# Optimization experiments

Measured on AMD Instinct MI355X. Metric: run time of the kernel, lower is better.

## Reference

```python
import jax, jax.numpy as jnp
import numpy as np

H = 128
N_CAN = 100000
N_FLAG = 50000
E = 600000
L = 500000


def _sage_conv(x_src, x_dst, edge_index, Wl, bl, Wr):
    # PyG SAGEConv (mean aggr): lin_l(mean_{j in N(i)} x_j) + lin_r(x_i)
    src, dst = edge_index[0], edge_index[1]
    msg = x_src[src]                                        # [E, H] gather
    n_dst = x_dst.shape[0]
    agg = jax.ops.segment_sum(msg, dst, num_segments=n_dst)  # [N_dst, H]
    cnt = jax.ops.segment_sum(jnp.ones((msg.shape[0],), msg.dtype), dst,
                              num_segments=n_dst)
    mean = agg / jnp.maximum(cnt, 1.0)[:, None]
    return mean @ Wl.T + bl + x_dst @ Wr.T


def setup_inputs() -> dict:
    key = jax.random.key(0)
    ks = jax.random.split(key, 16)
    s = 1.0 / np.sqrt(H)
    inp = {
        'can_node_id': jnp.arange(N_CAN, dtype=jnp.int64) if jax.config.jax_enable_x64 else jnp.arange(N_CAN, dtype=jnp.int32),
        'flag_node_id': jnp.arange(N_FLAG, dtype=jnp.int32),
        'edge_index_cf': jnp.stack([
            jax.random.randint(ks[0], (E,), 0, N_CAN),
            jax.random.randint(ks[1], (E,), 0, N_FLAG)]),
        'edge_index_fc': jnp.stack([
            jax.random.randint(ks[2], (E,), 0, N_FLAG),
            jax.random.randint(ks[3], (E,), 0, N_CAN)]),
        'edge_label_index': jnp.stack([
            jax.random.randint(ks[4], (L,), 0, N_CAN),
            jax.random.randint(ks[5], (L,), 0, N_FLAG)]),
        'can_emb': jax.random.normal(ks[6], (N_CAN, H), jnp.float32),
        'flag_emb': jax.random.normal(ks[7], (N_FLAG, H), jnp.float32),
        # SAGEConv for edge type CAN->flag (updates flag nodes)
        'Wl_cf': jax.random.normal(ks[8], (H, H), jnp.float32) * s,
        'bl_cf': jnp.zeros((H,), jnp.float32),
        'Wr_cf': jax.random.normal(ks[9], (H, H), jnp.float32) * s,
        # SAGEConv for edge type flag->CAN (updates CAN nodes)
        'Wl_fc': jax.random.normal(ks[10], (H, H), jnp.float32) * s,
        'bl_fc': jnp.zeros((H,), jnp.float32),
        'Wr_fc': jax.random.normal(ks[11], (H, H), jnp.float32) * s,
        # classifier MLP
        'W1': jax.random.normal(ks[12], (H, 2 * H), jnp.float32) * (1.0 / np.sqrt(2 * H)),
        'b1': jnp.zeros((H,), jnp.float32),
        'W2': jax.random.normal(ks[13], (1, H), jnp.float32) * s,
        'b2': jnp.zeros((1,), jnp.float32),
    }
    return inp


def reference(can_node_id, flag_node_id, edge_index_cf, edge_index_fc,
              edge_label_index, can_emb, flag_emb,
              Wl_cf, bl_cf, Wr_cf, Wl_fc, bl_fc, Wr_fc,
              W1, b1, W2, b2):
    # embedding lookups
    x_can = can_emb[can_node_id]    # [N_CAN, H]
    x_flag = flag_emb[flag_node_id]  # [N_FLAG, H]
    # to_hetero single SAGE layer + relu (dropout is identity in eval)
    upd_flag = jax.nn.relu(_sage_conv(x_can, x_flag, edge_index_cf, Wl_cf, bl_cf, Wr_cf))
    upd_can = jax.nn.relu(_sage_conv(x_flag, x_can, edge_index_fc, Wl_fc, bl_fc, Wr_fc))
    # link prediction classifier
    src = upd_can[edge_label_index[0]]   # [L, H]
    dst = upd_flag[edge_label_index[1]]  # [L, H]
    h = jax.nn.relu(jnp.concatenate([src, dst], axis=-1) @ W1.T + b1)
    out = h @ W2.T + b2
    return out.reshape(-1)
```

## Files before the change

### kernel.cpp

```cpp
#include <hip/hip_runtime.h>
#include <hip/hip_bf16.h>

#define H 128
#define BSH 8
#define MAXB 1024

typedef __attribute__((ext_vector_type(8))) short short8;
typedef __attribute__((ext_vector_type(4))) short short4v;
typedef __attribute__((ext_vector_type(4))) float floatx4;
typedef unsigned short ushort_t;
typedef unsigned int uint_t;

__device__ __forceinline__ short f2bf(float f) {
    __hip_bfloat16 h = __float2bfloat16(f);
    return *reinterpret_cast<short*>(&h);
}
__device__ __forceinline__ float bflo(uint_t u) { return __uint_as_float(u << 16); }
__device__ __forceinline__ float bfhi(uint_t u) { return __uint_as_float(u & 0xFFFF0000u); }
__device__ __forceinline__ uint_t pack_bf2(float x, float y) {
    return (uint_t)(ushort_t)f2bf(x) | ((uint_t)(ushort_t)f2bf(y) << 16);
}

__global__ __launch_bounds__(256)
void bucket_hist_cvt_kernel(const int* __restrict__ ei1, const int* __restrict__ ei2,
                            int E, int NF, int B, int* __restrict__ bcnt, int nbh,
                            const float* __restrict__ a, int n4a,
                            const float* __restrict__ b, int n4b,
                            ushort_t* __restrict__ da, ushort_t* __restrict__ db,
                            const float* __restrict__ Wl_cf, const float* __restrict__ Wr_cf,
                            const float* __restrict__ Wl_fc, const float* __restrict__ Wr_fc,
                            const float* __restrict__ W1, ushort_t* __restrict__ wb) {
    __shared__ int h[MAXB];
    int tid = threadIdx.x;
    if ((int)blockIdx.x < nbh) {
        for (int i = tid; i < B; i += 256) h[i] = 0;
        __syncthreads();
        int base = blockIdx.x * 4096;
        #pragma unroll 4
        for (int it = 0; it < 16; ++it) {
            int t = base + it * 256 + tid;
            if (t < 2 * E) {
                int g = (t < E) ? ei1[E + t] : (ei2[E + t - E] + NF);
                atomicAdd(&h[g >> BSH], 1);
            }
        }
        __syncthreads();
        for (int i = tid; i < B; i += 256)
            if (h[i]) atomicAdd(&bcnt[i], h[i]);
        return;
    }
    int i = ((int)blockIdx.x - nbh) * 256 + tid;
    const float* src; ushort_t* dst; int k;
    if (i < n4a) { src = a; dst = da; k = i; }
    else if (i < n4a + n4b) { src = b; dst = db; k = i - n4a; }
    else {
        int idx = (i - n4a - n4b) * 4;
        if (idx >= 98304) return;
        int off;
        if      (idx < 16384) { src = Wl_cf; off = idx; }
        else if (idx < 32768) { src = Wr_cf; off = idx - 16384; }
        else if (idx < 49152) { src = Wl_fc; off = idx - 32768; }
        else if (idx < 65536) { src = Wr_fc; off = idx - 49152; }
        else                  { src = W1;    off = idx - 65536; }
        float4 v = *(const float4*)(src + off);
        short4v s;
        s[0] = f2bf(v.x); s[1] = f2bf(v.y); s[2] = f2bf(v.z); s[3] = f2bf(v.w);
        *(short4v*)(wb + idx) = s;
        return;
    }
    float4 v = ((const float4*)src)[k];
    short4v s;
    s[0] = f2bf(v.x); s[1] = f2bf(v.y); s[2] = f2bf(v.z); s[3] = f2bf(v.w);
    ((short4v*)dst)[k] = s;
}

__global__ __launch_bounds__(256)
void bucket_scan_kernel(const int* __restrict__ bcnt, int B,
                        int* __restrict__ bbase, int* __restrict__ bfront) {
    __shared__ int sdata[256];
    int tid = threadIdx.x;
    int base = tid * 4;
    int v[4]; int s = 0;
    #pragma unroll
    for (int i = 0; i < 4; ++i) { int idx = base + i; v[i] = (idx < B) ? bcnt[idx] : 0; s += v[i]; }
    sdata[tid] = s;
    __syncthreads();
    for (int off = 1; off < 256; off <<= 1) {
        int t = (tid >= off) ? sdata[tid - off] : 0;
        __syncthreads();
        sdata[tid] += t;
        __syncthreads();
    }
    int excl = tid ? sdata[tid - 1] : 0;
    #pragma unroll
    for (int i = 0; i < 4; ++i) {
        int idx = base + i;
        if (idx < B) { bbase[idx] = excl; bfront[idx] = excl; }
        excl += v[i];
    }
    if (tid == 255) bbase[B] = excl;
}

__global__ __launch_bounds__(256)
void partition_kernel(const int* __restrict__ ei1, const int* __restrict__ ei2,
                      int E, int NF, int B,
                      int* __restrict__ bfront, uint2* __restrict__ part) {
    __shared__ int h[MAXB];
    __shared__ int basex[MAXB];
    int tid = threadIdx.x;
    for (int i = tid; i < B; i += 256) h[i] = 0;
    __syncthreads();
    int base = blockIdx.x * 4096;
    #pragma unroll 4
    for (int it = 0; it < 16; ++it) {
        int t = base + it * 256 + tid;
        if (t < 2 * E) {
            int g = (t < E) ? ei1[E + t] : (ei2[E + t - E] + NF);
            atomicAdd(&h[g >> BSH], 1);
        }
    }
    __syncthreads();
    for (int i = tid; i < B; i += 256) {
        int c = h[i];
        basex[i] = c ? atomicAdd(&bfront[i], c) : 0;
    }
    __syncthreads();
    for (int i = tid; i < B; i += 256) h[i] = 0;
    __syncthreads();
    #pragma unroll 4
    for (int it = 0; it < 16; ++it) {
        int t = base + it * 256 + tid;
        if (t < 2 * E) {
            int g, s;
            if (t < E) { g = ei1[E + t]; s = ei1[t]; }
            else       { int e = t - E; g = ei2[E + e] + NF; s = ei2[e]; }
            int bk = g >> BSH;
            int r = atomicAdd(&h[bk], 1);
            part[basex[bk] + r] = make_uint2((uint_t)s, (uint_t)g);
        }
    }
}

__global__ __launch_bounds__(256)
void fine_bin_kernel(const int* __restrict__ bbase, int nTot,
                     const uint2* __restrict__ part,
                     int* __restrict__ offs, int* __restrict__ bins) {
    __shared__ int cnt[256];
    __shared__ int sdata[256];
    __shared__ int excl[256];
    int b = blockIdx.x;
    int tid = threadIdx.x;
    int seg0 = bbase[b], seg1 = bbase[b + 1];
    int gbase = b << BSH;
    cnt[tid] = 0;
    __syncthreads();
    for (int k = seg0 + tid; k < seg1; k += 256)
        atomicAdd(&cnt[part[k].y - gbase], 1);
    __syncthreads();
    sdata[tid] = cnt[tid];
    __syncthreads();
    for (int off = 1; off < 256; off <<= 1) {
        int t = (tid >= off) ? sdata[tid - off] : 0;
        __syncthreads();
        sdata[tid] += t;
        __syncthreads();
    }
    excl[tid] = tid ? sdata[tid - 1] : 0;
    int g = gbase + tid;
    if (g < nTot) offs[g] = seg0 + excl[tid];
    if (b == (int)gridDim.x - 1 && tid == 0) offs[nTot] = seg1;
    cnt[tid] = 0;
    __syncthreads();
    for (int k = seg0 + tid; k < seg1; k += 256) {
        uint2 e = part[k];
        int l = (int)e.y - gbase;
        int r = atomicAdd(&cnt[l], 1);
        bins[seg0 + excl[l] + r] = (int)e.x;
    }
}

__global__ __launch_bounds__(256)
void gather_mean3_kernel(const int* __restrict__ offs, int nTotal, int split,
                         const int* __restrict__ bins,
                         const ushort_t* __restrict__ embA, ushort_t* __restrict__ aggA,
                         const ushort_t* __restrict__ embB, ushort_t* __restrict__ aggB) {
    int g = blockIdx.x * 4 + (threadIdx.x >> 6);
    if (g >= nTotal) return;
    int lane = threadIdx.x & 63;
    int q = lane >> 4, l15 = lane & 15;
    int start = offs[g];
    int end = offs[g + 1];
    int deg = end - start;
    const ushort_t* emb; ushort_t* agg; int row;
    if (g < split) { emb = embA; agg = aggA; row = g; }
    else           { emb = embB; agg = aggB; row = g - split; }

    float acc[8];
    #pragma unroll
    for (int t = 0; t < 8; ++t) acc[t] = 0.f;

    int nPre = deg < 64 ? deg : 64;
    int pre = (lane < nPre) ? bins[start + lane] : 0;

    int col = l15 * 8;
    for (int it = 0; it < (nPre + 7) / 8; ++it) {
        int e0 = 8 * it + q;
        int e1 = e0 + 4;
        int s0 = __shfl(pre, e0, 64);
        int s1 = __shfl(pre, e1, 64);
        if (e0 < nPre) {
            uint4 r = *(const uint4*)(emb + (size_t)s0 * H + col);
            acc[0] += bflo(r.x); acc[1] += bfhi(r.x);
            acc[2] += bflo(r.y); acc[3] += bfhi(r.y);
            acc[4] += bflo(r.z); acc[5] += bfhi(r.z);
            acc[6] += bflo(r.w); acc[7] += bfhi(r.w);
        }
        if (e1 < nPre) {
            uint4 r = *(const uint4*)(emb + (size_t)s1 * H + col);
            acc[0] += bflo(r.x); acc[1] += bfhi(r.x);
            acc[2] += bflo(r.y); acc[3] += bfhi(r.y);
            acc[4] += bflo(r.z); acc[5] += bfhi(r.z);
            acc[6] += bflo(r.w); acc[7] += bfhi(r.w);
        }
    }
    for (int k = start + 64 + q; k < end; k += 4) {
        int s = bins[k];
        uint4 r = *(const uint4*)(emb + (size_t)s * H + col);
        acc[0] += bflo(r.x); acc[1] += bfhi(r.x);
        acc[2] += bflo(r.y); acc[3] += bfhi(r.y);
        acc[4] += bflo(r.z); acc[5] += bfhi(r.z);
        acc[6] += bflo(r.w); acc[7] += bfhi(r.w);
    }

    #pragma unroll
    for (int t = 0; t < 8; ++t) {
        acc[t] += __shfl_xor(acc[t], 16, 64);
        acc[t] += __shfl_xor(acc[t], 32, 64);
    }
    if (q == 0) {
        float inv = 1.0f / fmaxf((float)deg, 1.0f);
        uint4 o;
        o.x = pack_bf2(acc[0] * inv, acc[1] * inv);
        o.y = pack_bf2(acc[2] * inv, acc[3] * inv);
        o.z = pack_bf2(acc[4] * inv, acc[5] * inv);
        o.w = pack_bf2(acc[6] * inv, acc[7] * inv);
        *(uint4*)(agg + (size_t)row * H + col) = o;
    }
}

__global__ __launch_bounds__(256)
void hist2_kernel(const int* __restrict__ ei1, const int* __restrict__ ei2, int E,
                  int* __restrict__ deg1, int* __restrict__ deg2) {
    int t = blockIdx.x * 256 + threadIdx.x;
    if (t < E) atomicAdd(&deg1[ei1[E + t]], 1);
    else if (t < 2 * E) { int e = t - E; atomicAdd(&deg2[ei2[E + e]], 1); }
}

__global__ __launch_bounds__(256)
void scan_blocksum_kernel(const int* __restrict__ deg, int n, int* __restrict__ bsums) {
    __shared__ int sdata[256];
    int tid = threadIdx.x;
    int base = blockIdx.x * 1024 + tid * 4;
    int v = 0;
    #pragma unroll
    for (int i = 0; i < 4; ++i) { int idx = base + i; if (idx < n) v += deg[idx]; }
    sdata[tid] = v;
    __syncthreads();
    for (int off = 128; off > 0; off >>= 1) {
        if (tid < off) sdata[tid] += sdata[tid + off];
        __syncthreads();
    }
    if (tid == 0) bsums[blockIdx.x] = sdata[0];
}

__global__ __launch_bounds__(256)
void scan_write_kernel(int* __restrict__ data, int n, const int* __restrict__ bsums) {
    __shared__ int sdata[256];
    __shared__ int boff;
    int tid = threadIdx.x;
    if (tid < 64) {
        int acc = 0;
        for (int i = tid; i < (int)blockIdx.x; i += 64) acc += bsums[i];
        #pragma unroll
        for (int off = 32; off > 0; off >>= 1) acc += __shfl_xor(acc, off, 64);
        if (tid == 0) boff = acc;
    }
    int base = blockIdx.x * 1024 + tid * 4;
    int v[4]; int s = 0;
    #pragma unroll
    for (int i = 0; i < 4; ++i) { int idx = base + i; v[i] = (idx < n) ? data[idx] : 0; s += v[i]; }
    sdata[tid] = s;
    __syncthreads();
    for (int off = 1; off < 256; off <<= 1) {
        int t = (tid >= off) ? sdata[tid - off] : 0;
        __syncthreads();
        sdata[tid] += t;
        __syncthreads();
    }
    int excl = (tid == 0 ? 0 : sdata[tid - 1]) + boff;
    #pragma unroll
    for (int i = 0; i < 4; ++i) {
        int idx = base + i;
        if (idx < n) data[idx] = excl;
        excl += v[i];
    }
}

__global__ __launch_bounds__(256)
void bin2_kernel(const int* __restrict__ ei1, const int* __restrict__ ei2, int E,
                 int* __restrict__ offs1, int* __restrict__ offs2,
                 int* __restrict__ bins) {
    int t = blockIdx.x * 256 + threadIdx.x;
    if (t < E) {
        int pos = atomicAdd(&offs1[ei1[E + t]], 1);
        bins[pos] = ei1[t];
    } else if (t < 2 * E) {
        int e = t - E;
        int pos = atomicAdd(&offs2[ei2[E + e]], 1);
        bins[pos] = ei2[e];
    }
}

__global__ __launch_bounds__(256)
void gather_mean2_incl_kernel(const int* __restrict__ offs, int nTotal, int split,
                              const int* __restrict__ bins,
                              const ushort_t* __restrict__ embA, ushort_t* __restrict__ aggA,
                              const ushort_t* __restrict__ embB, ushort_t* __restrict__ aggB) {
    int g = blockIdx.x * 4 + (threadIdx.x >> 6);
    if (g >= nTotal) return;
    int lane = threadIdx.x & 63;
    int q = lane >> 4, l15 = lane & 15;
    int end = offs[g];
    int start = (g == 0) ? 0 : offs[g - 1];
    int deg = end - start;
    const ushort_t* emb; ushort_t* agg; int row;
    if (g < split) { emb = embA; agg = aggA; row = g; }
    else           { emb = embB; agg = aggB; row = g - split; }
    float acc[8];
    #pragma unroll
    for (int t = 0; t < 8; ++t) acc[t] = 0.f;
    int nPre = deg < 64 ? deg : 64;
    int pre = (lane < nPre) ? bins[start + lane] : 0;
    int col = l15 * 8;
    for (int it = 0; it < (nPre + 7) / 8; ++it) {
        int e0 = 8 * it + q, e1 = e0 + 4;
        int s0 = __shfl(pre, e0, 64);
        int s1 = __shfl(pre, e1, 64);
        if (e0 < nPre) {
            uint4 r = *(const uint4*)(emb + (size_t)s0 * H + col);
            acc[0] += bflo(r.x); acc[1] += bfhi(r.x);
            acc[2] += bflo(r.y); acc[3] += bfhi(r.y);
            acc[4] += bflo(r.z); acc[5] += bfhi(r.z);
            acc[6] += bflo(r.w); acc[7] += bfhi(r.w);
        }
        if (e1 < nPre) {
            uint4 r = *(const uint4*)(emb + (size_t)s1 * H + col);
            acc[0] += bflo(r.x); acc[1] += bfhi(r.x);
            acc[2] += bflo(r.y); acc[3] += bfhi(r.y);
            acc[4] += bflo(r.z); acc[5] += bfhi(r.z);
            acc[6] += bflo(r.w); acc[7] += bfhi(r.w);
        }
    }
    for (int k = start + 64 + q; k < end; k += 4) {
        int s = bins[k];
        uint4 r = *(const uint4*)(emb + (size_t)s * H + col);
        acc[0] += bflo(r.x); acc[1] += bfhi(r.x);
        acc[2] += bflo(r.y); acc[3] += bfhi(r.y);
        acc[4] += bflo(r.z); acc[5] += bfhi(r.z);
        acc[6] += bflo(r.w); acc[7] += bfhi(r.w);
    }
    #pragma unroll
    for (int t = 0; t < 8; ++t) {
        acc[t] += __shfl_xor(acc[t], 16, 64);
        acc[t] += __shfl_xor(acc[t], 32, 64);
    }
    if (q == 0) {
        float inv = 1.0f / fmaxf((float)deg, 1.0f);
        uint4 o;
        o.x = pack_bf2(acc[0] * inv, acc[1] * inv);
        o.y = pack_bf2(acc[2] * inv, acc[3] * inv);
        o.z = pack_bf2(acc[4] * inv, acc[5] * inv);
        o.w = pack_bf2(acc[6] * inv, acc[7] * inv);
        *(uint4*)(agg + (size_t)row * H + col) = o;
    }
}

__global__ __launch_bounds__(256)
void sage2_kernel(int nbF, int NF, int NC,
                  ushort_t* __restrict__ aggf, const ushort_t* __restrict__ embf,
                  ushort_t* __restrict__ aggc, const ushort_t* __restrict__ embc,
                  const ushort_t* __restrict__ wlf, const ushort_t* __restrict__ wrf,
                  const float* __restrict__ blf,
                  const ushort_t* __restrict__ wlc, const ushort_t* __restrict__ wrc,
                  const float* __restrict__ blc,
                  const ushort_t* __restrict__ W1) {
    __shared__ short A[64][264];
    bool isF = (int)blockIdx.x < nbF;
    int nrows = isF ? NF : NC;
    int rbase = (isF ? blockIdx.x : blockIdx.x - nbF) * 64;
    ushort_t* io = isF ? aggf : aggc;
    const ushort_t* emb = isF ? embf : embc;
    const ushort_t* Wl = isF ? wlf : wlc;
    const ushort_t* Wr = isF ? wrf : wrc;
    const float* bl = isF ? blf : blc;
    int koff = isF ? 128 : 0;

    int tid = threadIdx.x;
    int lane = tid & 63;
    int wv = tid >> 6;
    int l15 = lane & 15;
    int quad = lane >> 4;
    int nb0 = 32 * wv + l15;

    for (int idx = tid; idx < 64 * 64; idx += 256) {
        int r = idx >> 6, qq = idx & 63;
        int row = rbase + r;
        short4v s = (short4v){0, 0, 0, 0};
        if (row < nrows) {
            const ushort_t* src = (qq < 32) ? (io + (size_t)row * H + qq * 4)
                                            : (emb + (size_t)row * H + (qq - 32) * 4);
            s = *(const short4v*)src;
        }
        *(short4v*)&A[r][qq * 4] = s;
    }

    floatx4 acc[4][2];
    #pragma unroll
    for (int i = 0; i < 4; ++i)
        #pragma unroll
        for (int j = 0; j < 2; ++j)
            acc[i][j] = (floatx4){0.f, 0.f, 0.f, 0.f};

    float blv0 = bl[nb0];
    float blv1 = bl[nb0 + 16];
    __syncthreads();

    #pragma unroll
    for (int half = 0; half < 2; ++half) {
        const ushort_t* W = half ? Wr : Wl;
        #pragma unroll
        for (int ks = 0; ks < 4; ++ks) {
            int kb = ks * 32 + quad * 8;
            short8 b0 = *(const short8*)(W + (size_t)nb0 * H + kb);
            short8 b1 = *(const short8*)(W + (size_t)(nb0 + 16) * H + kb);
            int ka = half * 128 + kb;
            #pragma unroll
            for (int mt = 0; mt < 4; ++mt) {
                short8 a = *(const short8*)&A[16 * mt + l15][ka];
                acc[mt][0] = __builtin_amdgcn_mfma_f32_16x16x32_bf16(a, b0, acc[mt][0], 0, 0, 0);
                acc[mt][1] = __builtin_amdgcn_mfma_f32_16x16x32_bf16(a, b1, acc[mt][1], 0, 0, 0);
            }
        }
    }

    __syncthreads();
    #pragma unroll
    for (int mt = 0; mt < 4; ++mt)
        #pragma unroll
        for (int nt = 0; nt < 2; ++nt) {
            float blv = nt ? blv1 : blv0;
            int colw = nb0 + 16 * nt;
            #pragma unroll
            for (int rg = 0; rg < 4; ++rg) {
                int row = 16 * mt + quad * 4 + rg;
                A[row][colw] = f2bf(fmaxf(acc[mt][nt][rg] + blv, 0.0f));
                acc[mt][nt][rg] = 0.0f;
            }
        }
    __syncthreads();

    const ushort_t* W1p = W1 + koff;
    #pragma unroll
    for (int ks = 0; ks < 4; ++ks) {
        int kb = ks * 32 + quad * 8;
        short8 b0 = *(const short8*)(W1p + (size_t)nb0 * 256 + kb);
        short8 b1 = *(const short8*)(W1p + (size_t)(nb0 + 16) * 256 + kb);
        #pragma unroll
        for (int mt = 0; mt < 4; ++mt) {
            short8 a = *(const short8*)&A[16 * mt + l15][kb];
            acc[mt][0] = __builtin_amdgcn_mfma_f32_16x16x32_bf16(a, b0, acc[mt][0], 0, 0, 0);
            acc[mt][1] = __builtin_amdgcn_mfma_f32_16x16x32_bf16(a, b1, acc[mt][1], 0, 0, 0);
        }
    }

    #pragma unroll
    for (int mt = 0; mt < 4; ++mt)
        #pragma unroll
        for (int rg = 0; rg < 4; ++rg) {
            int row = rbase + 16 * mt + quad * 4 + rg;
            if (row < nrows) {
                io[(size_t)row * H + nb0]      = (ushort_t)f2bf(acc[mt][0][rg]);
                io[(size_t)row * H + nb0 + 16] = (ushort_t)f2bf(acc[mt][1][rg]);
            }
        }
}

__global__ __launch_bounds__(256)
void classify_kernel(const int* __restrict__ eli, int L,
                     const ushort_t* __restrict__ u_can,
                     const ushort_t* __restrict__ u_flag,
                     const float* __restrict__ b1,
                     const float* __restrict__ W2,
                     const float* __restrict__ b2,
                     float* __restrict__ out) {
    int tid = threadIdx.x;
    int lane = tid & 63;
    int wv = tid >> 6;
    int sub = lane >> 4;
    int l15 = lane & 15;
    int p = blockIdx.x * 16 + wv * 4 + sub;
    if (p >= L) return;
    int i = eli[p];
    int j = eli[L + p];
    uint4 a = ((const uint4*)(u_can  + (size_t)i * H))[l15];
    uint4 b = ((const uint4*)(u_flag + (size_t)j * H))[l15];
    float4 bb0 = ((const float4*)b1)[l15 * 2];
    float4 bb1 = ((const float4*)b1)[l15 * 2 + 1];
    float4 w0  = ((const float4*)W2)[l15 * 2];
    float4 w1  = ((const float4*)W2)[l15 * 2 + 1];
    float s = fmaxf(bflo(a.x) + bflo(b.x) + bb0.x, 0.f) * w0.x
            + fmaxf(bfhi(a.x) + bfhi(b.x) + bb0.y, 0.f) * w0.y
            + fmaxf(bflo(a.y) + bflo(b.y) + bb0.z, 0.f) * w0.z
            + fmaxf(bfhi(a.y) + bfhi(b.y) + bb0.w, 0.f) * w0.w
            + fmaxf(bflo(a.z) + bflo(b.z) + bb1.x, 0.f) * w1.x
            + fmaxf(bfhi(a.z) + bfhi(b.z) + bb1.y, 0.f) * w1.y
            + fmaxf(bflo(a.w) + bflo(b.w) + bb1.z, 0.f) * w1.z
            + fmaxf(bfhi(a.w) + bfhi(b.w) + bb1.w, 0.f) * w1.w;
    #pragma unroll
    for (int off = 8; off > 0; off >>= 1)
        s += __shfl_down(s, off, 16);
    if (l15 == 0) out[p] = s + b2[0];
}

extern "C" void kernel_launch(void* const* d_in, const int* in_sizes, int n_in,
                              void* d_out, int out_size, void* d_ws, size_t ws_size,
                              hipStream_t stream) {
    const int*   ei_cf    = (const int*)d_in[2];
    const int*   ei_fc    = (const int*)d_in[3];
    const int*   eli      = (const int*)d_in[4];
    const float* can_emb  = (const float*)d_in[5];
    const float* flag_emb = (const float*)d_in[6];
    const float* Wl_cf    = (const float*)d_in[7];
    const float* bl_cf    = (const float*)d_in[8];
    const float* Wr_cf    = (const float*)d_in[9];
    const float* Wl_fc    = (const float*)d_in[10];
    const float* bl_fc    = (const float*)d_in[11];
    const float* Wr_fc    = (const float*)d_in[12];
    const float* W1       = (const float*)d_in[13];
    const float* b1       = (const float*)d_in[14];
    const float* W2       = (const float*)d_in[15];
    const float* b2       = (const float*)d_in[16];
    float* out = (float*)d_out;

    const int NCAN  = in_sizes[0];
    const int NFLAG = in_sizes[1];
    const int E     = in_sizes[2] / 2;
    const int L     = in_sizes[4] / 2;
    const int nTot  = NCAN + NFLAG;
    const int B     = (nTot + 255) >> BSH;

    ushort_t* aggc = (ushort_t*)d_ws;
    ushort_t* aggf = aggc + (size_t)NCAN * H;
    ushort_t* embc = aggf + (size_t)NFLAG * H;
    ushort_t* embf = embc + (size_t)NCAN * H;
    char* tail = (char*)(embf + (size_t)NFLAG * H);
    size_t tail_off = (size_t)(tail - (char*)d_ws);

    int nbF = (NFLAG + 63) / 64, nbC = (NCAN + 63) / 64;
    int n4c = NCAN * H / 4, n4f = NFLAG * H / 4;
    int nbcvt = (n4c + n4f + 24576 + 255) / 256;

    size_t off_offs  = tail_off;
    size_t off_bcnt  = off_offs  + (size_t)(nTot + 1) * 4;
    size_t off_bbase = off_bcnt  + (size_t)MAXB * 4;
    size_t off_bfrnt = off_bbase + (size_t)(MAXB + 1) * 4;
    size_t off_bins  = off_bfrnt + (size_t)MAXB * 4;
    size_t off_part  = (off_bins + (size_t)2 * E * 4 + 7) & ~(size_t)7;
    size_t off_wb    = off_part + (size_t)2 * E * 8;
    size_t need_new  = off_wb + 98304 * 2;

    if (ws_size >= need_new && B <= MAXB) {
        int* offs   = (int*)((char*)d_ws + off_offs);
        int* bcnt   = (int*)((char*)d_ws + off_bcnt);
        int* bbase  = (int*)((char*)d_ws + off_bbase);
        int* bfront = (int*)((char*)d_ws + off_bfrnt);
        int* bins   = (int*)((char*)d_ws + off_bins);
        uint2* part = (uint2*)((char*)d_ws + off_part);
        ushort_t* wb = (ushort_t*)((char*)d_ws + off_wb);
        ushort_t* wb_wlcf = wb, *wb_wrcf = wb + 16384, *wb_wlfc = wb + 32768,
                 *wb_wrfc = wb + 49152, *wb_w1 = wb + 65536;

        int nbh = (2 * E + 4095) >> 12;
        hipMemsetAsync(bcnt, 0, (size_t)MAXB * 4, stream);
        bucket_hist_cvt_kernel<<<nbh + nbcvt, 256, 0, stream>>>(
            ei_cf, ei_fc, E, NFLAG, B, bcnt, nbh,
            can_emb, n4c, flag_emb, n4f, embc, embf,
            Wl_cf, Wr_cf, Wl_fc, Wr_fc, W1, wb);
        bucket_scan_kernel<<<1, 256, 0, stream>>>(bcnt, B, bbase, bfront);
        partition_kernel<<<nbh, 256, 0, stream>>>(ei_cf, ei_fc, E, NFLAG, B, bfront, part);
        fine_bin_kernel<<<B, 256, 0, stream>>>(bbase, nTot, part, offs, bins);
        gather_mean3_kernel<<<(nTot + 3) / 4, 256, 0, stream>>>(
            offs, nTot, NFLAG, bins, embc, aggf, embf, aggc);
        sage2_kernel<<<nbF + nbC, 256, 0, stream>>>(
            nbF, NFLAG, NCAN, aggf, embf, aggc, embc,
            wb_wlcf, wb_wrcf, bl_cf, wb_wlfc, wb_wrfc, bl_fc, wb_w1);
    } else {
        int* scanf_ = (int*)tail;
        int* scanc_ = scanf_ + NFLAG;
        int* bins   = scanc_ + NCAN;
        int* bsums  = bins + 2 * E;
        ushort_t* wb = (ushort_t*)(bsums + 256);
        ushort_t* wb_wlcf = wb, *wb_wrcf = wb + 16384, *wb_wlfc = wb + 32768,
                 *wb_wrfc = wb + 49152, *wb_w1 = wb + 65536;

        bucket_hist_cvt_kernel<<<nbcvt, 256, 0, stream>>>(
            ei_cf, ei_fc, E, NFLAG, B, (int*)tail , 0,
            can_emb, n4c, flag_emb, n4f, embc, embf,
            Wl_cf, Wr_cf, Wl_fc, Wr_fc, W1, wb);
        hipMemsetAsync(scanf_, 0, ((size_t)NFLAG + NCAN) * 4, stream);
        int nb = (nTot + 1023) / 1024;
        hist2_kernel<<<(2 * E + 255) / 256, 256, 0, stream>>>(ei_cf, ei_fc, E, scanf_, scanc_);
        scan_blocksum_kernel<<<nb, 256, 0, stream>>>(scanf_, nTot, bsums);
        scan_write_kernel<<<nb, 256, 0, stream>>>(scanf_, nTot, bsums);
        bin2_kernel<<<(2 * E + 255) / 256, 256, 0, stream>>>(ei_cf, ei_fc, E, scanf_, scanc_, bins);
        gather_mean2_incl_kernel<<<(nTot + 3) / 4, 256, 0, stream>>>(
            scanf_, nTot, NFLAG, bins, embc, aggf, embf, aggc);
        sage2_kernel<<<nbF + nbC, 256, 0, stream>>>(
            nbF, NFLAG, NCAN, aggf, embf, aggc, embc,
            wb_wlcf, wb_wrcf, bl_cf, wb_wlfc, wb_wrfc, bl_fc, wb_w1);
    }

    classify_kernel<<<(L + 15) / 16, 256, 0, stream>>>(
        eli, L, aggc, aggf, b1, W2, b2, out);
}
```

Baseline: 343.4 us.

## Fold bucket scan into partition kernels and pack partition entries into 32 bits

Removes the single-block bucket_scan kernel: partition_kernel and fine_bin_kernel now each compute the bucket prefix sums they need directly from the bucket counts. Partition entries shrink from an 8-byte (src, dst) pair to one 32-bit word holding the 8-bit local bucket offset and a 24-bit source index, which halves partition traffic. The fallback path is reworked to share gather_mean3 through a new conversion kernel. The cost is redundant per-block scan work, and the packing assumes source indices fit in 24 bits.

New measurement: 341.1 us. No clear change (-0.7%).

```diff
diff --git a/kernel.cpp b/kernel.cpp
--- a/kernel.cpp
+++ b/kernel.cpp
@@ -75,39 +75,34 @@
 }
 
 __global__ __launch_bounds__(256)
-void bucket_scan_kernel(const int* __restrict__ bcnt, int B,
-                        int* __restrict__ bbase, int* __restrict__ bfront) {
-    __shared__ int sdata[256];
-    int tid = threadIdx.x;
-    int base = tid * 4;
-    int v[4]; int s = 0;
-    #pragma unroll
-    for (int i = 0; i < 4; ++i) { int idx = base + i; v[i] = (idx < B) ? bcnt[idx] : 0; s += v[i]; }
-    sdata[tid] = s;
-    __syncthreads();
-    for (int off = 1; off < 256; off <<= 1) {
-        int t = (tid >= off) ? sdata[tid - off] : 0;
-        __syncthreads();
-        sdata[tid] += t;
-        __syncthreads();
-    }
-    int excl = tid ? sdata[tid - 1] : 0;
-    #pragma unroll
-    for (int i = 0; i < 4; ++i) {
-        int idx = base + i;
-        if (idx < B) { bbase[idx] = excl; bfront[idx] = excl; }
-        excl += v[i];
-    }
-    if (tid == 255) bbase[B] = excl;
-}
-
-__global__ __launch_bounds__(256)
 void partition_kernel(const int* __restrict__ ei1, const int* __restrict__ ei2,
-                      int E, int NF, int B,
-                      int* __restrict__ bfront, uint2* __restrict__ part) {
+                      int E, int NF, int B, const int* __restrict__ bcnt,
+                      int* __restrict__ bfront, uint_t* __restrict__ part) {
     __shared__ int h[MAXB];
     __shared__ int basex[MAXB];
-    int tid = threadIdx.x;
+    __shared__ int sdata[256];
+    int tid = threadIdx.x;
+    {
+        int base4 = tid * 4;
+        int v[4]; int s = 0;
+        #pragma unroll
+        for (int i = 0; i < 4; ++i) { int idx = base4 + i; v[i] = (idx < B) ? bcnt[idx] : 0; s += v[i]; }
+        sdata[tid] = s;
+        __syncthreads();
+        for (int off = 1; off < 256; off <<= 1) {
+            int t = (tid >= off) ? sdata[tid - off] : 0;
+            __syncthreads();
+            sdata[tid] += t;
+            __syncthreads();
+        }
+        int excl = tid ? sdata[tid - 1] : 0;
+        #pragma unroll
+        for (int i = 0; i < 4; ++i) {
+            int idx = base4 + i;
+            if (idx < B) basex[idx] = excl;
+            excl += v[i];
+        }
+    }
     for (int i = tid; i < B; i += 256) h[i] = 0;
     __syncthreads();
     int base = blockIdx.x * 4096;
@@ -122,7 +117,7 @@
     __syncthreads();
     for (int i = tid; i < B; i += 256) {
         int c = h[i];
-        basex[i] = c ? atomicAdd(&bfront[i], c) : 0;
+        if (c) basex[i] += atomicAdd(&bfront[i], c);
     }
     __syncthreads();
     for (int i = tid; i < B; i += 256) h[i] = 0;
@@ -136,26 +131,38 @@
             else       { int e = t - E; g = ei2[E + e] + NF; s = ei2[e]; }
             int bk = g >> BSH;
             int r = atomicAdd(&h[bk], 1);
-            part[basex[bk] + r] = make_uint2((uint_t)s, (uint_t)g);
-        }
-    }
-}
-
-__global__ __launch_bounds__(256)
-void fine_bin_kernel(const int* __restrict__ bbase, int nTot,
-                     const uint2* __restrict__ part,
+            part[basex[bk] + r] = ((uint_t)(g & 255) << 24) | (uint_t)s;
+        }
+    }
+}
+
+__global__ __launch_bounds__(256)
+void fine_bin_kernel(const int* __restrict__ bcnt, int B, int nTot, int E2,
+                     const uint_t* __restrict__ part,
                      int* __restrict__ offs, int* __restrict__ bins) {
     __shared__ int cnt[256];
     __shared__ int sdata[256];
     __shared__ int excl[256];
     int b = blockIdx.x;
     int tid = threadIdx.x;
-    int seg0 = bbase[b], seg1 = bbase[b + 1];
+    {
+        int partial = 0;
+        for (int i = tid; i < b; i += 256) partial += bcnt[i];
+        sdata[tid] = partial;
+        __syncthreads();
+        for (int off = 128; off > 0; off >>= 1) {
+            if (tid < off) sdata[tid] += sdata[tid + off];
+            __syncthreads();
+        }
+    }
+    int seg0 = sdata[0];
+    int seg1 = seg0 + bcnt[b];
     int gbase = b << BSH;
+    __syncthreads();
     cnt[tid] = 0;
     __syncthreads();
     for (int k = seg0 + tid; k < seg1; k += 256)
-        atomicAdd(&cnt[part[k].y - gbase], 1);
+        atomicAdd(&cnt[part[k] >> 24], 1);
     __syncthreads();
     sdata[tid] = cnt[tid];
     __syncthreads();
@@ -168,14 +175,14 @@
     excl[tid] = tid ? sdata[tid - 1] : 0;
     int g = gbase + tid;
     if (g < nTot) offs[g] = seg0 + excl[tid];
-    if (b == (int)gridDim.x - 1 && tid == 0) offs[nTot] = seg1;
+    if (b == 0 && tid == 0) offs[nTot] = E2;
     cnt[tid] = 0;
     __syncthreads();
     for (int k = seg0 + tid; k < seg1; k += 256) {
-        uint2 e = part[k];
-        int l = (int)e.y - gbase;
+        uint_t e = part[k];
+        int l = (int)(e >> 24);
         int r = atomicAdd(&cnt[l], 1);
-        bins[seg0 + excl[l] + r] = (int)e.x;
+        bins[seg0 + excl[l] + r] = (int)(e & 0x00FFFFFFu);
     }
 }
 
@@ -232,143 +239,6 @@
         acc[6] += bflo(r.w); acc[7] += bfhi(r.w);
     }
 
-    #pragma unroll
-    for (int t = 0; t < 8; ++t) {
-        acc[t] += __shfl_xor(acc[t], 16, 64);
-        acc[t] += __shfl_xor(acc[t], 32, 64);
-    }
-    if (q == 0) {
-        float inv = 1.0f / fmaxf((float)deg, 1.0f);
-        uint4 o;
-        o.x = pack_bf2(acc[0] * inv, acc[1] * inv);
-        o.y = pack_bf2(acc[2] * inv, acc[3] * inv);
-        o.z = pack_bf2(acc[4] * inv, acc[5] * inv);
-        o.w = pack_bf2(acc[6] * inv, acc[7] * inv);
-        *(uint4*)(agg + (size_t)row * H + col) = o;
-    }
-}
-
-__global__ __launch_bounds__(256)
-void hist2_kernel(const int* __restrict__ ei1, const int* __restrict__ ei2, int E,
-                  int* __restrict__ deg1, int* __restrict__ deg2) {
-    int t = blockIdx.x * 256 + threadIdx.x;
-    if (t < E) atomicAdd(&deg1[ei1[E + t]], 1);
-    else if (t < 2 * E) { int e = t - E; atomicAdd(&deg2[ei2[E + e]], 1); }
-}
-
-__global__ __launch_bounds__(256)
-void scan_blocksum_kernel(const int* __restrict__ deg, int n, int* __restrict__ bsums) {
-    __shared__ int sdata[256];
-    int tid = threadIdx.x;
-    int base = blockIdx.x * 1024 + tid * 4;
-    int v = 0;
-    #pragma unroll
-    for (int i = 0; i < 4; ++i) { int idx = base + i; if (idx < n) v += deg[idx]; }
-    sdata[tid] = v;
-    __syncthreads();
-    for (int off = 128; off > 0; off >>= 1) {
-        if (tid < off) sdata[tid] += sdata[tid + off];
-        __syncthreads();
-    }
-    if (tid == 0) bsums[blockIdx.x] = sdata[0];
-}
-
-__global__ __launch_bounds__(256)
-void scan_write_kernel(int* __restrict__ data, int n, const int* __restrict__ bsums) {
-    __shared__ int sdata[256];
-    __shared__ int boff;
-    int tid = threadIdx.x;
-    if (tid < 64) {
-        int acc = 0;
-        for (int i = tid; i < (int)blockIdx.x; i += 64) acc += bsums[i];
-        #pragma unroll
-        for (int off = 32; off > 0; off >>= 1) acc += __shfl_xor(acc, off, 64);
-        if (tid == 0) boff = acc;
-    }
-    int base = blockIdx.x * 1024 + tid * 4;
-    int v[4]; int s = 0;
-    #pragma unroll
-    for (int i = 0; i < 4; ++i) { int idx = base + i; v[i] = (idx < n) ? data[idx] : 0; s += v[i]; }
-    sdata[tid] = s;
-    __syncthreads();
-    for (int off = 1; off < 256; off <<= 1) {
-        int t = (tid >= off) ? sdata[tid - off] : 0;
-        __syncthreads();
-        sdata[tid] += t;
-        __syncthreads();
-    }
-    int excl = (tid == 0 ? 0 : sdata[tid - 1]) + boff;
-    #pragma unroll
-    for (int i = 0; i < 4; ++i) {
-        int idx = base + i;
-        if (idx < n) data[idx] = excl;
-        excl += v[i];
-    }
-}
-
-__global__ __launch_bounds__(256)
-void bin2_kernel(const int* __restrict__ ei1, const int* __restrict__ ei2, int E,
-                 int* __restrict__ offs1, int* __restrict__ offs2,
-                 int* __restrict__ bins) {
-    int t = blockIdx.x * 256 + threadIdx.x;
-    if (t < E) {
-        int pos = atomicAdd(&offs1[ei1[E + t]], 1);
-        bins[pos] = ei1[t];
-    } else if (t < 2 * E) {
-        int e = t - E;
-        int pos = atomicAdd(&offs2[ei2[E + e]], 1);
-        bins[pos] = ei2[e];
-    }
-}
-
-__global__ __launch_bounds__(256)
-void gather_mean2_incl_kernel(const int* __restrict__ offs, int nTotal, int split,
-                              const int* __restrict__ bins,
-                              const ushort_t* __restrict__ embA, ushort_t* __restrict__ aggA,
-                              const ushort_t* __restrict__ embB, ushort_t* __restrict__ aggB) {
-    int g = blockIdx.x * 4 + (threadIdx.x >> 6);
-    if (g >= nTotal) return;
-    int lane = threadIdx.x & 63;
-    int q = lane >> 4, l15 = lane & 15;
-    int end = offs[g];
-    int start = (g == 0) ? 0 : offs[g - 1];
-    int deg = end - start;
-    const ushort_t* emb; ushort_t* agg; int row;
-    if (g < split) { emb = embA; agg = aggA; row = g; }
-    else           { emb = embB; agg = aggB; row = g - split; }
-    float acc[8];
-    #pragma unroll
-    for (int t = 0; t < 8; ++t) acc[t] = 0.f;
-    int nPre = deg < 64 ? deg : 64;
-    int pre = (lane < nPre) ? bins[start + lane] : 0;
-    int col = l15 * 8;
-    for (int it = 0; it < (nPre + 7) / 8; ++it) {
-        int e0 = 8 * it + q, e1 = e0 + 4;
-        int s0 = __shfl(pre, e0, 64);
-        int s1 = __shfl(pre, e1, 64);
-        if (e0 < nPre) {
-            uint4 r = *(const uint4*)(emb + (size_t)s0 * H + col);
-            acc[0] += bflo(r.x); acc[1] += bfhi(r.x);
-            acc[2] += bflo(r.y); acc[3] += bfhi(r.y);
-            acc[4] += bflo(r.z); acc[5] += bfhi(r.z);
-            acc[6] += bflo(r.w); acc[7] += bfhi(r.w);
-        }
-        if (e1 < nPre) {
-            uint4 r = *(const uint4*)(emb + (size_t)s1 * H + col);
-            acc[0] += bflo(r.x); acc[1] += bfhi(r.x);
-            acc[2] += bflo(r.y); acc[3] += bfhi(r.y);
-            acc[4] += bflo(r.z); acc[5] += bfhi(r.z);
-            acc[6] += bflo(r.w); acc[7] += bfhi(r.w);
-        }
-    }
-    for (int k = start + 64 + q; k < end; k += 4) {
-        int s = bins[k];
-        uint4 r = *(const uint4*)(emb + (size_t)s * H + col);
-        acc[0] += bflo(r.x); acc[1] += bfhi(r.x);
-        acc[2] += bflo(r.y); acc[3] += bfhi(r.y);
-        acc[4] += bflo(r.z); acc[5] += bfhi(r.z);
-        acc[6] += bflo(r.w); acc[7] += bfhi(r.w);
-    }
     #pragma unroll
     for (int t = 0; t < 8; ++t) {
         acc[t] += __shfl_xor(acc[t], 16, 64);
@@ -493,6 +363,86 @@
                 io[(size_t)row * H + nb0 + 16] = (ushort_t)f2bf(acc[mt][1][rg]);
             }
         }
+}
+
+__global__ __launch_bounds__(256)
+void hist2_kernel(const int* __restrict__ ei1, const int* __restrict__ ei2, int E,
+                  int* __restrict__ deg1, int* __restrict__ deg2) {
+    int t = blockIdx.x * 256 + threadIdx.x;
+    if (t < E) atomicAdd(&deg1[ei1[E + t]], 1);
+    else if (t < 2 * E) { int e = t - E; atomicAdd(&deg2[ei2[E + e]], 1); }
+}
+
+__global__ __launch_bounds__(256)
+void scan_blocksum_kernel(const int* __restrict__ deg, int n, int* __restrict__ bsums) {
+    __shared__ int sdata[256];
+    int tid = threadIdx.x;
+    int base = blockIdx.x * 1024 + tid * 4;
+    int v = 0;
+    #pragma unroll
+    for (int i = 0; i < 4; ++i) { int idx = base + i; if (idx < n) v += deg[idx]; }
+    sdata[tid] = v;
+    __syncthreads();
+    for (int off = 128; off > 0; off >>= 1) {
+        if (tid < off) sdata[tid] += sdata[tid + off];
+        __syncthreads();
+    }
+    if (tid == 0) bsums[blockIdx.x] = sdata[0];
+}
+
+__global__ __launch_bounds__(256)
+void scan_write_kernel(int* __restrict__ data, int n, const int* __restrict__ bsums) {
+    __shared__ int sdata[256];
+    __shared__ int boff;
+    int tid = threadIdx.x;
+    if (tid < 64) {
+        int acc = 0;
+        for (int i = tid; i < (int)blockIdx.x; i += 64) acc += bsums[i];
+        #pragma unroll
+        for (int off = 32; off > 0; off >>= 1) acc += __shfl_xor(acc, off, 64);
+        if (tid == 0) boff = acc;
+    }
+    int base = blockIdx.x * 1024 + tid * 4;
+    int v[4]; int s = 0;
+    #pragma unroll
+    for (int i = 0; i < 4; ++i) { int idx = base + i; v[i] = (idx < n) ? data[idx] : 0; s += v[i]; }
+    sdata[tid] = s;
+    __syncthreads();
+    for (int off = 1; off < 256; off <<= 1) {
+        int t = (tid >= off) ? sdata[tid - off] : 0;
+        __syncthreads();
+        sdata[tid] += t;
+        __syncthreads();
+    }
+    int excl = (tid == 0 ? 0 : sdata[tid - 1]) + boff;
+    #pragma unroll
+    for (int i = 0; i < 4; ++i) {
+        int idx = base + i;
+        if (idx < n) data[idx] = excl;
+        excl += v[i];
+    }
+}
+
+__global__ __launch_bounds__(256)
+void incl_to_start_kernel(const int* __restrict__ incl, int nTot, int* __restrict__ offs) {
+    int g = blockIdx.x * 256 + threadIdx.x;
+    if (g < nTot) offs[g + 1] = incl[g];
+    if (g == 0) offs[0] = 0;
+}
+
+__global__ __launch_bounds__(256)
+void bin2_kernel(const int* __restrict__ ei1, const int* __restrict__ ei2, int E,
+                 int* __restrict__ offs1, int* __restrict__ offs2,
+                 int* __restrict__ bins) {
+    int t = blockIdx.x * 256 + threadIdx.x;
+    if (t < E) {
+        int pos = atomicAdd(&offs1[ei1[E + t]], 1);
+        bins[pos] = ei1[t];
+    } else if (t < 2 * E) {
+        int e = t - E;
+        int pos = atomicAdd(&offs2[ei2[E + e]], 1);
+        bins[pos] = ei2[e];
+    }
 }
 
 __global__ __launch_bounds__(256)
@@ -572,49 +522,47 @@
 
     size_t off_offs  = tail_off;
     size_t off_bcnt  = off_offs  + (size_t)(nTot + 1) * 4;
-    size_t off_bbase = off_bcnt  + (size_t)MAXB * 4;
-    size_t off_bfrnt = off_bbase + (size_t)(MAXB + 1) * 4;
+    size_t off_bfrnt = off_bcnt  + (size_t)MAXB * 4;
     size_t off_bins  = off_bfrnt + (size_t)MAXB * 4;
-    size_t off_part  = (off_bins + (size_t)2 * E * 4 + 7) & ~(size_t)7;
-    size_t off_wb    = off_part + (size_t)2 * E * 8;
+    size_t off_part  = off_bins  + (size_t)2 * E * 4;
+    size_t off_wb    = off_part  + (size_t)2 * E * 4;
     size_t need_new  = off_wb + 98304 * 2;
 
+    int* offs   = (int*)((char*)d_ws + off_offs);
+    int* bcnt   = (int*)((char*)d_ws + off_bcnt);
+    int* bfront = (int*)((char*)d_ws + off_bfrnt);
+    int* bins   = (int*)((char*)d_ws + off_bins);
+
     if (ws_size >= need_new && B <= MAXB) {
-        int* offs   = (int*)((char*)d_ws + off_offs);
-        int* bcnt   = (int*)((char*)d_ws + off_bcnt);
-        int* bbase  = (int*)((char*)d_ws + off_bbase);
-        int* bfront = (int*)((char*)d_ws + off_bfrnt);
-        int* bins   = (int*)((char*)d_ws + off_bins);
-        uint2* part = (uint2*)((char*)d_ws + off_part);
+        uint_t* part = (uint_t*)((char*)d_ws + off_part);
         ushort_t* wb = (ushort_t*)((char*)d_ws + off_wb);
         ushort_t* wb_wlcf = wb, *wb_wrcf = wb + 16384, *wb_wlfc = wb + 32768,
                  *wb_wrfc = wb + 49152, *wb_w1 = wb + 65536;
 
         int nbh = (2 * E + 4095) >> 12;
-        hipMemsetAsync(bcnt, 0, (size_t)MAXB * 4, stream);
+        hipMemsetAsync(bcnt, 0, (size_t)2 * MAXB * 4, stream);
         bucket_hist_cvt_kernel<<<nbh + nbcvt, 256, 0, stream>>>(
             ei_cf, ei_fc, E, NFLAG, B, bcnt, nbh,
             can_emb, n4c, flag_emb, n4f, embc, embf,
             Wl_cf, Wr_cf, Wl_fc, Wr_fc, W1, wb);
-        bucket_scan_kernel<<<1, 256, 0, stream>>>(bcnt, B, bbase, bfront);
-        partition_kernel<<<nbh, 256, 0, stream>>>(ei_cf, ei_fc, E, NFLAG, B, bfront, part);
-        fine_bin_kernel<<<B, 256, 0, stream>>>(bbase, nTot, part, offs, bins);
+        partition_kernel<<<nbh, 256, 0, stream>>>(ei_cf, ei_fc, E, NFLAG, B, bcnt, bfront, part);
+        fine_bin_kernel<<<B, 256, 0, stream>>>(bcnt, B, nTot, 2 * E, part, offs, bins);
         gather_mean3_kernel<<<(nTot + 3) / 4, 256, 0, stream>>>(
             offs, nTot, NFLAG, bins, embc, aggf, embf, aggc);
         sage2_kernel<<<nbF + nbC, 256, 0, stream>>>(
             nbF, NFLAG, NCAN, aggf, embf, aggc, embc,
             wb_wlcf, wb_wrcf, bl_cf, wb_wlfc, wb_wrfc, bl_fc, wb_w1);
     } else {
-        int* scanf_ = (int*)tail;
+        int* scanf_ = bins;
         int* scanc_ = scanf_ + NFLAG;
-        int* bins   = scanc_ + NCAN;
-        int* bsums  = bins + 2 * E;
+        int* bins2  = scanc_ + NCAN;
+        int* bsums  = bins2 + 2 * E;
         ushort_t* wb = (ushort_t*)(bsums + 256);
         ushort_t* wb_wlcf = wb, *wb_wrcf = wb + 16384, *wb_wlfc = wb + 32768,
                  *wb_wrfc = wb + 49152, *wb_w1 = wb + 65536;
 
         bucket_hist_cvt_kernel<<<nbcvt, 256, 0, stream>>>(
-            ei_cf, ei_fc, E, NFLAG, B, (int*)tail , 0,
+            ei_cf, ei_fc, E, NFLAG, B, bcnt, 0,
             can_emb, n4c, flag_emb, n4f, embc, embf,
             Wl_cf, Wr_cf, Wl_fc, Wr_fc, W1, wb);
         hipMemsetAsync(scanf_, 0, ((size_t)NFLAG + NCAN) * 4, stream);
@@ -622,9 +570,10 @@
         hist2_kernel<<<(2 * E + 255) / 256, 256, 0, stream>>>(ei_cf, ei_fc, E, scanf_, scanc_);
         scan_blocksum_kernel<<<nb, 256, 0, stream>>>(scanf_, nTot, bsums);
         scan_write_kernel<<<nb, 256, 0, stream>>>(scanf_, nTot, bsums);
-        bin2_kernel<<<(2 * E + 255) / 256, 256, 0, stream>>>(ei_cf, ei_fc, E, scanf_, scanc_, bins);
-        gather_mean2_incl_kernel<<<(nTot + 3) / 4, 256, 0, stream>>>(
-            scanf_, nTot, NFLAG, bins, embc, aggf, embf, aggc);
+        bin2_kernel<<<(2 * E + 255) / 256, 256, 0, stream>>>(ei_cf, ei_fc, E, scanf_, scanc_, bins2);
+        incl_to_start_kernel<<<(nTot + 255) / 256, 256, 0, stream>>>(scanf_, nTot, offs);
+        gather_mean3_kernel<<<(nTot + 3) / 4, 256, 0, stream>>>(
+            offs, nTot, NFLAG, bins2, embc, aggf, embf, aggc);
         sage2_kernel<<<nbF + nbC, 256, 0, stream>>>(
             nbF, NFLAG, NCAN, aggf, embf, aggc, embc,
             wb_wlcf, wb_wrcf, bl_cf, wb_wlfc, wb_wrfc, bl_fc, wb_w1);
```
